# Kernel optimization log

Measured on AMD Instinct MI355X. Metric: run time of the kernel, lower is better.

The kernel has to match this reference:

```python
import jax, jax.numpy as jnp
import numpy as np
import math

EPS = 1e-07
ALPHA = 0.2
FINAL_LAMBDA = 0.01   # final_beta in the original
ITERATIONS = 2
MEAN_DATA = 1.0

B, H, W, KH, KW, I, O, A = 16, 6, 6, 3, 3, 32, 32, 4


def setup_inputs() -> dict:
    key = jax.random.key(0)
    k1, k2 = jax.random.split(key)
    votes = jax.random.normal(k1, (B, H, W, KH, KW, I, O, A, A), dtype=jnp.float32)
    activations = jax.random.uniform(k2, (B, H, W, KH, KW, I, 1, 1, 1), dtype=jnp.float32)
    beta_a = jnp.full((1, 1, 1, 1, 1, 1, O, 1, 1), 0.5, dtype=jnp.float32)
    beta_u = jnp.full((1, 1, 1, 1, 1, 1, O, 1, 1), 0.5, dtype=jnp.float32)
    return {"votes": votes, "activations": activations, "beta_a": beta_a, "beta_u": beta_u}


def _m_step(a_i, V, R, R_prev, beta_a, beta_u, it_idx):
    # R mixing with previous assignments (faithful to source)
    R = R * a_i * (1.0 - ALPHA) + ALPHA * R_prev
    R_prev = R
    # reduce over kernel (3,4) and input-capsule (5) axes
    sum_R = jnp.sum(R, axis=(3, 4, 5), keepdims=True)                      # (b,h,w,1,1,1,o,1,1)
    mu = jnp.sum(R * V, axis=(3, 4, 5), keepdims=True) / (sum_R + EPS)     # (b,h,w,1,1,1,o,a,a)
    sigma_sq = jnp.sum(R * (V - mu) ** 2, axis=(3, 4, 5), keepdims=True) / (sum_R + EPS)
    cost_h = (beta_u - 0.5 * jnp.log(sigma_sq + EPS)) * sum_R / MEAN_DATA
    inv_temp = FINAL_LAMBDA * (1.0 - 0.95 ** (it_idx + 1))
    a_j = jax.nn.sigmoid(inv_temp * (beta_a - jnp.sum(cost_h, axis=(-1, -2), keepdims=True)))
    return mu, sigma_sq, a_j, R_prev


def _e_step_log(V, mu, sigma_sq, a_j):
    # log-space E-step: log N(V; mu, sigma) summed over the 4x4 pose entries
    log_p = -jnp.sum(jnp.log(2.0 * math.pi * sigma_sq + EPS) + (V - mu) ** 2 / (2.0 * sigma_sq),
                     axis=(-1, -2), keepdims=True)                         # (b,h,w,kh,kw,i,o,1,1)
    log_num = jnp.log(a_j + EPS) + log_p
    log_den = jax.scipy.special.logsumexp(log_num, axis=(3, 4, 6), keepdims=True)
    return jnp.exp(log_num - log_den)


def reference(votes, activations, beta_a, beta_u):
    b, h, w, kh, kw, i, o, a, _ = votes.shape
    # softmax over zeros along axis 6 -> uniform 1/o
    R = jnp.full((b, h, w, 1, 1, i, o, 1, 1), 1.0 / o, dtype=votes.dtype)
    R_prev = R
    mu = sigma_sq = a_j = None
    for it in range(ITERATIONS - 1):
        mu, sigma_sq, a_j, R_prev = _m_step(activations, votes, R, R_prev, beta_a, beta_u, it)
        R = _e_step_log(votes, mu, sigma_sq, a_j)
    # final M-step called with i = iterations (matches source)
    mu, sigma_sq, a_j, R_prev = _m_step(activations, votes, R, R_prev, beta_a, beta_u, ITERATIONS)
    poses = jnp.squeeze(mu, axis=(3, 4, 5))   # (b,h,w,o,a,a)
    acts = jnp.squeeze(a_j, axis=(3, 4, 5))   # (b,h,w,o,1,1)
    return poses, acts
```

## Files before the change

### kernel.cpp

```cpp
#include <hip/hip_runtime.h>


#define KKc 9
#define NIc 32
#define NOc 32
#define NAc 16
#define KIc 288
#define NPc 512
#define NSITE 576
#define RSTR 20

#define EPSf 1e-7f
#define TWO_PIf 6.28318530717958647692f

__device__ __forceinline__ float wave_sum(float v) {
#pragma unroll
  for (int off = 32; off; off >>= 1) v += __shfl_down(v, off, 64);
  return v;
}
__device__ __forceinline__ float wave_max(float v) {
#pragma unroll
  for (int off = 32; off; off >>= 1) v = fmaxf(v, __shfl_down(v, off, 64));
  return v;
}

__global__ __launch_bounds__(128)
void em_k1(const float* __restrict__ votes, const float* __restrict__ acts_in,
           const float* __restrict__ beta_a, const float* __restrict__ beta_u,
           float* __restrict__ w_mu1, float* __restrict__ w_i2s,
           float* __restrict__ w_m1v, float* __restrict__ w_m1q,
           float* __restrict__ w_base, float* __restrict__ w_sR1)
{
  const int site = blockIdx.x >> 2;
  const int qtr  = blockIdx.x & 3;
  const int t    = threadIdx.x;

  __shared__ float s_act[KIc];
  __shared__ float s_red[2];
  __shared__ float s_cr[32 * 9];

  s_act[t] = acts_in[site * KIc + t];
  s_act[t + 128] = acts_in[site * KIc + t + 128];
  if (t < 32) s_act[t + 256] = acts_in[site * KIc + t + 256];
  __syncthreads();

  float v = fmaf(0.8f, s_act[t], 0.2f) + fmaf(0.8f, s_act[t + 128], 0.2f);
  if (t < 32) v += fmaf(0.8f, s_act[t + 256], 0.2f);
  v = wave_sum(v);
  if ((t & 63) == 0) s_red[t >> 6] = v;
  __syncthreads();
  const float sumR1 = (s_red[0] + s_red[1]) * 0.03125f;

  const int c  = qtr * 32 + (t & 31);
  const int r0 = t >> 5;
  float pv0 = 0.f, pv1 = 0.f, pv2 = 0.f, pv3 = 0.f;
  float pq0 = 0.f, pq1 = 0.f, pq2 = 0.f, pq3 = 0.f;
  const float4* vb = reinterpret_cast<const float4*>(votes) + (size_t)site * (KIc * 128) + c;
#pragma unroll 8
  for (int k = 0; k < 72; ++k) {
    const int ki = r0 + 4 * k;
    const float r = fmaf(0.8f, s_act[ki], 0.2f) * 0.03125f;
    const float4 x = vb[(size_t)ki * 128];
    pv0 = fmaf(r, x.x, pv0); pq0 = fmaf(r, x.x * x.x, pq0);
    pv1 = fmaf(r, x.y, pv1); pq1 = fmaf(r, x.y * x.y, pq1);
    pv2 = fmaf(r, x.z, pv2); pq2 = fmaf(r, x.z * x.z, pq2);
    pv3 = fmaf(r, x.w, pv3); pq3 = fmaf(r, x.w * x.w, pq3);
  }
  pv0 += __shfl_xor(pv0, 32); pv1 += __shfl_xor(pv1, 32);
  pv2 += __shfl_xor(pv2, 32); pv3 += __shfl_xor(pv3, 32);
  pq0 += __shfl_xor(pq0, 32); pq1 += __shfl_xor(pq1, 32);
  pq2 += __shfl_xor(pq2, 32); pq3 += __shfl_xor(pq3, 32);
  if (t >= 64 && t < 96) {
    const int l = t - 64;
    s_cr[l * 9 + 0] = pv0; s_cr[l * 9 + 1] = pv1; s_cr[l * 9 + 2] = pv2; s_cr[l * 9 + 3] = pv3;
    s_cr[l * 9 + 4] = pq0; s_cr[l * 9 + 5] = pq1; s_cr[l * 9 + 6] = pq2; s_cr[l * 9 + 7] = pq3;
  }
  __syncthreads();
  if (t < 32) {
    pv0 += s_cr[t * 9 + 0]; pv1 += s_cr[t * 9 + 1]; pv2 += s_cr[t * 9 + 2]; pv3 += s_cr[t * 9 + 3];
    pq0 += s_cr[t * 9 + 4]; pq1 += s_cr[t * 9 + 5]; pq2 += s_cr[t * 9 + 6]; pq3 += s_cr[t * 9 + 7];

    const float sR1e = sumR1 + EPSf;
    const float sR1x = sumR1 + 2.f * EPSf;
    const float mu0 = pv0 / sR1e, mu1 = pv1 / sR1e, mu2 = pv2 / sR1e, mu3 = pv3 / sR1e;
    const float sg0 = fmaxf((pq0 - mu0 * mu0 * sR1x) / sR1e, 0.f);
    const float sg1 = fmaxf((pq1 - mu1 * mu1 * sR1x) / sR1e, 0.f);
    const float sg2 = fmaxf((pq2 - mu2 * mu2 * sR1x) / sR1e, 0.f);
    const float sg3 = fmaxf((pq3 - mu3 * mu3 * sR1x) / sR1e, 0.f);

    const size_t fo = (size_t)site * 128 + c;
    reinterpret_cast<float4*>(w_mu1)[fo] = make_float4(mu0, mu1, mu2, mu3);
    reinterpret_cast<float4*>(w_i2s)[fo] = make_float4(0.5f / sg0, 0.5f / sg1, 0.5f / sg2, 0.5f / sg3);
    reinterpret_cast<float4*>(w_m1v)[fo] = make_float4(pv0, pv1, pv2, pv3);
    reinterpret_cast<float4*>(w_m1q)[fo] = make_float4(pq0, pq1, pq2, pq3);

    const int o = c >> 2;
    const float bu = beta_u[o];
    float lt = logf(TWO_PIf * sg0 + EPSf) + logf(TWO_PIf * sg1 + EPSf)
             + logf(TWO_PIf * sg2 + EPSf) + logf(TWO_PIf * sg3 + EPSf);
    float ch = (4.f * bu - 0.5f * (logf(sg0 + EPSf) + logf(sg1 + EPSf)
                                 + logf(sg2 + EPSf) + logf(sg3 + EPSf))) * sumR1;
    ch += __shfl_xor(ch, 1); ch += __shfl_xor(ch, 2);
    lt += __shfl_xor(lt, 1); lt += __shfl_xor(lt, 2);
    if ((t & 3) == 0) {
      const float aj = 1.f / (1.f + expf(-(0.0005f * (beta_a[o] - ch))));
      w_base[site * NOc + o] = logf(aj + EPSf) - lt;
    }
    if (t == 0) w_sR1[site] = sumR1;
  }
}

__global__ __launch_bounds__(256)
void em_k3(const float* __restrict__ votes, const float* __restrict__ acts_in,
           const float* __restrict__ w_mu1, const float* __restrict__ w_i2s,
           const float* __restrict__ w_base, float* __restrict__ w_part)
{
  const int site = (NSITE - 1) - (blockIdx.x >> 3);
  const int ig   = blockIdx.x & 7;
  const int t    = threadIdx.x;
  const int o    = t & 31;

  __shared__ float s_V[288 * RSTR];
  __shared__ float s_act[KIc];
  __shared__ float s_base[NOc];
  __shared__ float s_rm[4];
  __shared__ float s_re[4];

  {
    const int tt = t & 127;
    const float4 x = reinterpret_cast<const float4*>((t < 128 ? w_mu1 : w_i2s) + (size_t)site * NPc)[tt];
    float* dst = s_V + (t < 128 ? 0 : 544) + (tt >> 2) * 17 + (tt & 3) * 4;
    dst[0] = x.x; dst[1] = x.y; dst[2] = x.z; dst[3] = x.w;
  }
  s_act[t] = acts_in[site * KIc + t];
  if (t < 32) { s_act[256 + t] = acts_in[site * KIc + 256 + t]; s_base[t] = w_base[site * NOc + t]; }
  __syncthreads();
  float mu[16], is[16];
#pragma unroll
  for (int a = 0; a < 16; ++a) { mu[a] = s_V[o * 17 + a]; is[a] = s_V[544 + o * 17 + a]; }
  const float lbase = s_base[o];
  __syncthreads();

  float accv[16], accq[16], accw = 0.f;
#pragma unroll
  for (int a = 0; a < 16; ++a) { accv[a] = 0.f; accq[a] = 0.f; }

  const float4* vsl4 = reinterpret_cast<const float4*>(votes) + (size_t)site * (KIc * 128);

  for (int ii = 0; ii < 4; ++ii) {
    const int i = ig * 4 + ii;
#pragma unroll
    for (int idx = t; idx < 1152; idx += 256) {
      const int row = idx >> 2;
      const int a4  = idx & 3;
      const float4 x = vsl4[(size_t)((row >> 5) * NIc + i) * 128 + (row & 31) * 4 + a4];
      *reinterpret_cast<float4*>(s_V + row * RSTR + a4 * 4) = x;
    }
    __syncthreads();

    float v1[16];
#pragma unroll
    for (int j = 0; j < 4; ++j) {
      const float4 x = *reinterpret_cast<const float4*>(s_V + t * RSTR + 4 * j);
      v1[4 * j] = x.x; v1[4 * j + 1] = x.y; v1[4 * j + 2] = x.z; v1[4 * j + 3] = x.w;
    }
    float lp1 = 0.f;
#pragma unroll
    for (int a = 0; a < 16; ++a) { const float d = v1[a] - mu[a]; lp1 = fmaf(d * d, is[a], lp1); }
    const float ln1 = lbase - lp1;

    float v2[16];
    float ln2 = -1e30f;
    if (t < 32) {
#pragma unroll
      for (int j = 0; j < 4; ++j) {
        const float4 x = *reinterpret_cast<const float4*>(s_V + (256 + t) * RSTR + 4 * j);
        v2[4 * j] = x.x; v2[4 * j + 1] = x.y; v2[4 * j + 2] = x.z; v2[4 * j + 3] = x.w;
      }
      float lp2 = 0.f;
#pragma unroll
      for (int a = 0; a < 16; ++a) { const float d = v2[a] - mu[a]; lp2 = fmaf(d * d, is[a], lp2); }
      ln2 = lbase - lp2;
    }

    float m = wave_max(fmaxf(ln1, ln2));
    if ((t & 63) == 0) s_rm[t >> 6] = m;
    __syncthreads();
    m = fmaxf(fmaxf(s_rm[0], s_rm[1]), fmaxf(s_rm[2], s_rm[3]));
    float e = expf(ln1 - m) + ((t < 32) ? expf(ln2 - m) : 0.f);
    e = wave_sum(e);
    if ((t & 63) == 0) s_re[t >> 6] = e;
    __syncthreads();
    const float logden = m + logf(s_re[0] + s_re[1] + s_re[2] + s_re[3]);

    const float w1 = expf(ln1 - logden) * s_act[(t >> 5) * NIc + i] * 0.8f;
    accw += w1;
#pragma unroll
    for (int a = 0; a < 16; ++a) {
      accv[a] = fmaf(w1, v1[a], accv[a]);
      accq[a] = fmaf(w1, v1[a] * v1[a], accq[a]);
    }
    if (t < 32) {
      const float w2 = expf(ln2 - logden) * s_act[8 * NIc + i] * 0.8f;
      accw += w2;
#pragma unroll
      for (int a = 0; a < 16; ++a) {
        accv[a] = fmaf(w2, v2[a], accv[a]);
        accq[a] = fmaf(w2, v2[a] * v2[a], accq[a]);
      }
    }
  }

  accw += __shfl_xor(accw, 32);
#pragma unroll
  for (int a = 0; a < 16; ++a) {
    accv[a] += __shfl_xor(accv[a], 32);
    accq[a] += __shfl_xor(accq[a], 32);
  }
  float* s_p = s_V;
  {
    const int l = t & 63, wv = t >> 6;
    if (l < 32) {
#pragma unroll
      for (int a = 0; a < 16; ++a) {
        s_p[a * 128 + wv * 32 + l] = accv[a];
        s_p[(16 + a) * 128 + wv * 32 + l] = accq[a];
      }
      s_p[32 * 128 + wv * 32 + l] = accw;
    }
  }
  __syncthreads();
  float* wp = w_part + (size_t)(site * 8 + ig) * (33 * 32);
  for (int j = t >> 5; j < 33; j += 8) {
    const float s = s_p[j * 128 + o] + s_p[j * 128 + 32 + o]
                  + s_p[j * 128 + 64 + o] + s_p[j * 128 + 96 + o];
    wp[j * 32 + o] = s;
  }
}

__global__ __launch_bounds__(256)
void em_k4(const float* __restrict__ beta_a, const float* __restrict__ beta_u,
           const float* __restrict__ w_m1v, const float* __restrict__ w_m1q,
           const float* __restrict__ w_sR1, const float* __restrict__ w_part,
           float* __restrict__ out)
{
  const int site = blockIdx.x;
  const int t    = threadIdx.x;
  const int oB   = t & 31;
  const int a2B  = (t >> 5) * 2;

  __shared__ float s_M[33 * 32];
  __shared__ float s_c[256];

  for (int j = t >> 5; j < 33; j += 8) {
    float s = 0.f;
#pragma unroll
    for (int g = 0; g < 8; ++g)
      s += w_part[(size_t)(site * 8 + g) * (33 * 32) + j * 32 + oB];
    s_M[j * 32 + oB] = s;
  }
  __syncthreads();

  const float sumR1 = w_sR1[site];
  const float sumR  = s_M[32 * 32 + oB] + 0.2f * sumR1;
  const float sRe   = sumR + EPSf;
  const float sRx   = sumR + 2.f * EPSf;
  const int p = oB * NAc + a2B;

  const float Mva = s_M[a2B * 32 + oB]        + 0.2f * w_m1v[(size_t)site * NPc + p];
  const float Mvb = s_M[(a2B + 1) * 32 + oB]  + 0.2f * w_m1v[(size_t)site * NPc + p + 1];
  const float Mqa = s_M[(16 + a2B) * 32 + oB] + 0.2f * w_m1q[(size_t)site * NPc + p];
  const float Mqb = s_M[(17 + a2B) * 32 + oB] + 0.2f * w_m1q[(size_t)site * NPc + p + 1];

  const float mua = Mva / sRe;
  const float mub = Mvb / sRe;
  const float sga = fmaxf((Mqa - mua * mua * sRx) / sRe, 0.f);
  const float sgb = fmaxf((Mqb - mub * mub * sRx) / sRe, 0.f);

  reinterpret_cast<float2*>(out + (size_t)site * NPc)[p >> 1] = make_float2(mua, mub);

  const float bu = beta_u[oB];
  s_c[t] = (bu - 0.5f * logf(sga + EPSf)) * sumR
         + (bu - 0.5f * logf(sgb + EPSf)) * sumR;
  __syncthreads();
  if (t < NOc) {
    float c = 0.f;
#pragma unroll
    for (int k = 0; k < 8; ++k) c += s_c[t + 32 * k];
    const float aj = 1.f / (1.f + expf(-(0.00142625f * (beta_a[t] - c))));
    out[(size_t)NSITE * NPc + site * NOc + t] = aj;
  }
}

extern "C" void kernel_launch(void* const* d_in, const int* in_sizes, int n_in,
                              void* d_out, int out_size, void* d_ws, size_t ws_size,
                              hipStream_t stream) {
  const float* votes  = (const float*)d_in[0];
  const float* acts   = (const float*)d_in[1];
  const float* beta_a = (const float*)d_in[2];
  const float* beta_u = (const float*)d_in[3];
  float* out = (float*)d_out;

  float* ws = (float*)d_ws;
  const size_t SP = (size_t)NSITE * NPc;
  float* w_mu1  = ws;
  float* w_i2s  = ws + SP;
  float* w_m1v  = ws + 2 * SP;
  float* w_m1q  = ws + 3 * SP;
  float* w_base = ws + 4 * SP;
  float* w_sR1  = w_base + NSITE * NOc;
  float* w_part = w_sR1 + 1024;

  em_k1<<<NSITE * 4, 128, 0, stream>>>(votes, acts, beta_a, beta_u,
                                       w_mu1, w_i2s, w_m1v, w_m1q, w_base, w_sR1);
  em_k3<<<NSITE * 8, 256, 0, stream>>>(votes, acts, w_mu1, w_i2s, w_base, w_part);
  em_k4<<<NSITE, 256, 0, stream>>>(beta_a, beta_u, w_m1v, w_m1q, w_sR1, w_part, out);
}
```

Baseline: 552.5 us.

## Load votes directly from global in em_k3 and merge softmax reductions

em_k3 no longer stages each input capsule's vote slice in shared memory. Each thread now reads its own 16-float vote row straight from global memory, and the second-kernel-position row is re-read from global instead of being kept in registers. The two-pass block max/sum for the log-sum-exp is replaced by one per-wave max plus rescaled sum, combined through a double-buffered shared array, so each iteration needs one barrier instead of three. This cuts shared memory use and synchronisation and may raise occupancy. The cost is uncoalesced-stride float4 global loads and a duplicate read of the second vote row.

```diff
diff --git a/kernel.cpp b/kernel.cpp
--- a/kernel.cpp
+++ b/kernel.cpp
@@ -8,7 +8,6 @@
 #define KIc 288
 #define NPc 512
 #define NSITE 576
-#define RSTR 20
 
 #define EPSf 1e-7f
 #define TWO_PIf 6.28318530717958647692f
@@ -18,9 +17,9 @@
   for (int off = 32; off; off >>= 1) v += __shfl_down(v, off, 64);
   return v;
 }
-__device__ __forceinline__ float wave_max(float v) {
-#pragma unroll
-  for (int off = 32; off; off >>= 1) v = fmaxf(v, __shfl_down(v, off, 64));
+__device__ __forceinline__ float wave_max_all(float v) {
+#pragma unroll
+  for (int off = 32; off; off >>= 1) v = fmaxf(v, __shfl_xor(v, off, 64));
   return v;
 }
 
@@ -119,81 +118,87 @@
   const int ig   = blockIdx.x & 7;
   const int t    = threadIdx.x;
   const int o    = t & 31;
-
-  __shared__ float s_V[288 * RSTR];
+  const int kk   = t >> 5;
+
   __shared__ float s_act[KIc];
-  __shared__ float s_base[NOc];
-  __shared__ float s_rm[4];
-  __shared__ float s_re[4];
-
+  __shared__ float s_lse[2][8];
+  __shared__ float s_p[33 * 128];
+
+  s_act[t] = acts_in[site * KIc + t];
+  if (t < 32) s_act[256 + t] = acts_in[site * KIc + 256 + t];
+
+  float mu[16], is[16];
   {
-    const int tt = t & 127;
-    const float4 x = reinterpret_cast<const float4*>((t < 128 ? w_mu1 : w_i2s) + (size_t)site * NPc)[tt];
-    float* dst = s_V + (t < 128 ? 0 : 544) + (tt >> 2) * 17 + (tt & 3) * 4;
-    dst[0] = x.x; dst[1] = x.y; dst[2] = x.z; dst[3] = x.w;
-  }
-  s_act[t] = acts_in[site * KIc + t];
-  if (t < 32) { s_act[256 + t] = acts_in[site * KIc + 256 + t]; s_base[t] = w_base[site * NOc + t]; }
-  __syncthreads();
-  float mu[16], is[16];
-#pragma unroll
-  for (int a = 0; a < 16; ++a) { mu[a] = s_V[o * 17 + a]; is[a] = s_V[544 + o * 17 + a]; }
-  const float lbase = s_base[o];
-  __syncthreads();
+    const float4* mp = reinterpret_cast<const float4*>(w_mu1 + (size_t)site * NPc) + o * 4;
+    const float4* ip = reinterpret_cast<const float4*>(w_i2s + (size_t)site * NPc) + o * 4;
+#pragma unroll
+    for (int j = 0; j < 4; ++j) {
+      const float4 a = mp[j];
+      mu[4 * j] = a.x; mu[4 * j + 1] = a.y; mu[4 * j + 2] = a.z; mu[4 * j + 3] = a.w;
+      const float4 b = ip[j];
+      is[4 * j] = b.x; is[4 * j + 1] = b.y; is[4 * j + 2] = b.z; is[4 * j + 3] = b.w;
+    }
+  }
+  const float lbase = w_base[site * NOc + o];
 
   float accv[16], accq[16], accw = 0.f;
 #pragma unroll
   for (int a = 0; a < 16; ++a) { accv[a] = 0.f; accq[a] = 0.f; }
 
-  const float4* vsl4 = reinterpret_cast<const float4*>(votes) + (size_t)site * (KIc * 128);
+  const float4* vrow = reinterpret_cast<const float4*>(votes)
+                     + (size_t)site * (KIc * 128) + o * 4;
 
   for (int ii = 0; ii < 4; ++ii) {
     const int i = ig * 4 + ii;
-#pragma unroll
-    for (int idx = t; idx < 1152; idx += 256) {
-      const int row = idx >> 2;
-      const int a4  = idx & 3;
-      const float4 x = vsl4[(size_t)((row >> 5) * NIc + i) * 128 + (row & 31) * 4 + a4];
-      *reinterpret_cast<float4*>(s_V + row * RSTR + a4 * 4) = x;
-    }
-    __syncthreads();
 
     float v1[16];
-#pragma unroll
-    for (int j = 0; j < 4; ++j) {
-      const float4 x = *reinterpret_cast<const float4*>(s_V + t * RSTR + 4 * j);
-      v1[4 * j] = x.x; v1[4 * j + 1] = x.y; v1[4 * j + 2] = x.z; v1[4 * j + 3] = x.w;
+    {
+      const float4* p1 = vrow + (size_t)(kk * NIc + i) * 128;
+#pragma unroll
+      for (int j = 0; j < 4; ++j) {
+        const float4 x = p1[j];
+        v1[4 * j] = x.x; v1[4 * j + 1] = x.y; v1[4 * j + 2] = x.z; v1[4 * j + 3] = x.w;
+      }
     }
     float lp1 = 0.f;
 #pragma unroll
     for (int a = 0; a < 16; ++a) { const float d = v1[a] - mu[a]; lp1 = fmaf(d * d, is[a], lp1); }
     const float ln1 = lbase - lp1;
 
-    float v2[16];
     float ln2 = -1e30f;
     if (t < 32) {
+      const float4* p2 = vrow + (size_t)(8 * NIc + i) * 128;
+      float lp2 = 0.f;
 #pragma unroll
       for (int j = 0; j < 4; ++j) {
-        const float4 x = *reinterpret_cast<const float4*>(s_V + (256 + t) * RSTR + 4 * j);
-        v2[4 * j] = x.x; v2[4 * j + 1] = x.y; v2[4 * j + 2] = x.z; v2[4 * j + 3] = x.w;
+        const float4 x = p2[j];
+        float d;
+        d = x.x - mu[4 * j];     lp2 = fmaf(d * d, is[4 * j],     lp2);
+        d = x.y - mu[4 * j + 1]; lp2 = fmaf(d * d, is[4 * j + 1], lp2);
+        d = x.z - mu[4 * j + 2]; lp2 = fmaf(d * d, is[4 * j + 2], lp2);
+        d = x.w - mu[4 * j + 3]; lp2 = fmaf(d * d, is[4 * j + 3], lp2);
       }
-      float lp2 = 0.f;
-#pragma unroll
-      for (int a = 0; a < 16; ++a) { const float d = v2[a] - mu[a]; lp2 = fmaf(d * d, is[a], lp2); }
       ln2 = lbase - lp2;
     }
 
-    float m = wave_max(fmaxf(ln1, ln2));
-    if ((t & 63) == 0) s_rm[t >> 6] = m;
+    const float mw = wave_max_all(fmaxf(ln1, ln2));
+    float e = expf(ln1 - mw) + ((t < 32) ? expf(ln2 - mw) : 0.f);
+    e = wave_sum(e);
+    if ((t & 63) == 0) {
+      s_lse[ii & 1][(t >> 6) * 2 + 0] = mw;
+      s_lse[ii & 1][(t >> 6) * 2 + 1] = e;
+    }
     __syncthreads();
-    m = fmaxf(fmaxf(s_rm[0], s_rm[1]), fmaxf(s_rm[2], s_rm[3]));
-    float e = expf(ln1 - m) + ((t < 32) ? expf(ln2 - m) : 0.f);
-    e = wave_sum(e);
-    if ((t & 63) == 0) s_re[t >> 6] = e;
-    __syncthreads();
-    const float logden = m + logf(s_re[0] + s_re[1] + s_re[2] + s_re[3]);
-
-    const float w1 = expf(ln1 - logden) * s_act[(t >> 5) * NIc + i] * 0.8f;
+    const float m0 = s_lse[ii & 1][0], e0 = s_lse[ii & 1][1];
+    const float m1 = s_lse[ii & 1][2], e1 = s_lse[ii & 1][3];
+    const float m2 = s_lse[ii & 1][4], e2 = s_lse[ii & 1][5];
+    const float m3 = s_lse[ii & 1][6], e3 = s_lse[ii & 1][7];
+    const float gm = fmaxf(fmaxf(m0, m1), fmaxf(m2, m3));
+    const float den = e0 * expf(m0 - gm) + e1 * expf(m1 - gm)
+                    + e2 * expf(m2 - gm) + e3 * expf(m3 - gm);
+    const float logden = gm + logf(den);
+
+    const float w1 = expf(ln1 - logden) * s_act[kk * NIc + i] * 0.8f;
     accw += w1;
 #pragma unroll
     for (int a = 0; a < 16; ++a) {
@@ -203,10 +208,18 @@
     if (t < 32) {
       const float w2 = expf(ln2 - logden) * s_act[8 * NIc + i] * 0.8f;
       accw += w2;
-#pragma unroll
-      for (int a = 0; a < 16; ++a) {
-        accv[a] = fmaf(w2, v2[a], accv[a]);
-        accq[a] = fmaf(w2, v2[a] * v2[a], accq[a]);
+      const float4* p2 = vrow + (size_t)(8 * NIc + i) * 128;
+#pragma unroll
+      for (int j = 0; j < 4; ++j) {
+        const float4 x = p2[j];
+        accv[4 * j]     = fmaf(w2, x.x, accv[4 * j]);
+        accq[4 * j]     = fmaf(w2, x.x * x.x, accq[4 * j]);
+        accv[4 * j + 1] = fmaf(w2, x.y, accv[4 * j + 1]);
+        accq[4 * j + 1] = fmaf(w2, x.y * x.y, accq[4 * j + 1]);
+        accv[4 * j + 2] = fmaf(w2, x.z, accv[4 * j + 2]);
+        accq[4 * j + 2] = fmaf(w2, x.z * x.z, accq[4 * j + 2]);
+        accv[4 * j + 3] = fmaf(w2, x.w, accv[4 * j + 3]);
+        accq[4 * j + 3] = fmaf(w2, x.w * x.w, accq[4 * j + 3]);
       }
     }
   }
@@ -217,7 +230,6 @@
     accv[a] += __shfl_xor(accv[a], 32);
     accq[a] += __shfl_xor(accq[a], 32);
   }
-  float* s_p = s_V;
   {
     const int l = t & 63, wv = t >> 6;
     if (l < 32) {
```

New measurement: 516.6 us. 1.07x faster.
